# Optimization experiments

Measured on AMD Instinct MI355X. Metric: run time of the kernel, lower is better.

## Reference

```python
import jax, jax.numpy as jnp
import numpy as np

NEG_SLOPE = 0.2  # PyG GATConv default negative_slope


def gat_conv(x, edge_index, W, a_src, a_dst, b):
    """PyG GATConv with add_self_loops=True, concat=False (mean over heads).
    x: [N, F_in]; W: [F_in, H*D]; a_src/a_dst: [H, D]; b: [D].
    Returns [N, D].
    """
    N = x.shape[0]
    H, D = a_src.shape
    xh = (x @ W).reshape(N, H, D)            # [N, H, D]
    loop = jnp.arange(N, dtype=edge_index.dtype)
    src = jnp.concatenate([edge_index[0], loop])  # [E+N]
    dst = jnp.concatenate([edge_index[1], loop])  # [E+N]
    # per-node attention logits
    asrc = jnp.einsum('nhd,hd->nh', xh, a_src)    # [N, H]
    adst = jnp.einsum('nhd,hd->nh', xh, a_dst)    # [N, H]
    e = asrc[src] + adst[dst]                      # [E+N, H]
    e = jnp.where(e > 0, e, NEG_SLOPE * e)         # LeakyReLU
    # softmax over incoming edges of each destination node
    emax = jax.ops.segment_max(e, dst, num_segments=N)   # [N, H]
    ex = jnp.exp(e - emax[dst])
    denom = jax.ops.segment_sum(ex, dst, num_segments=N) # [N, H]
    alpha = ex / denom[dst]                               # [E+N, H]
    # scatter-aggregate messages
    out = jax.ops.segment_sum(alpha[:, :, None] * xh[src], dst, num_segments=N)  # [N, H, D]
    return out.mean(axis=1) + b                           # concat=False -> mean heads


def setup_inputs() -> dict:
    key = jax.random.key(0)
    ks = jax.random.split(key, 10)
    N, F, D, C, H, E = 100000, 128, 32, 16, 8, 1600000
    s1 = 1.0 / np.sqrt(F)
    s2 = 1.0 / np.sqrt(D)
    return {
        'x': jax.random.normal(ks[0], (N, F), dtype=jnp.float32),
        'edge_index': jax.random.randint(ks[1], (2, E), 0, N, dtype=jnp.int32),
        'W1': jax.random.normal(ks[2], (F, H * D), dtype=jnp.float32) * s1,
        'a_src1': jax.random.normal(ks[3], (H, D), dtype=jnp.float32) * s2,
        'a_dst1': jax.random.normal(ks[4], (H, D), dtype=jnp.float32) * s2,
        'b1': jnp.zeros((D,), dtype=jnp.float32),
        'W2': jax.random.normal(ks[5], (D, H * C), dtype=jnp.float32) * s2,
        'a_src2': jax.random.normal(ks[6], (H, C), dtype=jnp.float32) * (1.0 / np.sqrt(C)),
        'a_dst2': jax.random.normal(ks[7], (H, C), dtype=jnp.float32) * (1.0 / np.sqrt(C)),
        'b2': jnp.zeros((C,), dtype=jnp.float32),
    }


def reference(x, edge_index, W1, a_src1, a_dst1, b1, W2, a_src2, a_dst2, b2):
    h = gat_conv(x, edge_index, W1, a_src1, a_dst1, b1)
    h = jax.nn.elu(h)                       # F.elu; Dropout(p=0.0) is identity
    logits = gat_conv(h, edge_index, W2, a_src2, a_dst2, b2)
    return (jax.nn.log_softmax(logits, axis=1), logits)
```

## Files before the change

### kernel.cpp

```cpp
#include <hip/hip_runtime.h>
#include <hip/hip_bf16.h>
#include <hip/hip_fp16.h>
#include <math.h>

#define LEAK 0.2f
#define BSTRIDE 64

typedef _Float16 f16;
typedef _Float16 f16x2 __attribute__((ext_vector_type(2)));
typedef _Float16 f16x4 __attribute__((ext_vector_type(4)));
typedef _Float16 f16x8 __attribute__((ext_vector_type(8)));
typedef float f32x2 __attribute__((ext_vector_type(2)));
typedef float f32x4 __attribute__((ext_vector_type(4)));

__device__ inline unsigned char f32_to_fp8(float v) {
  int p = __builtin_amdgcn_cvt_pk_fp8_f32(v, v, 0, false);
  return (unsigned char)(p & 0xff);
}

__global__ void transpose_w_k(const float* __restrict__ W, f16* __restrict__ Wt,
                              int K, int NC) {
  int idx = blockIdx.x * 256 + threadIdx.x;
  if (idx >= K * NC) return;
  int n = idx / K, k = idx - n * K;
  Wt[idx] = (f16)W[(size_t)k * NC + n];
}

template <int K, int DH, bool FP8OUT, bool FILL>
__global__ __launch_bounds__(256) void gemm_att_mfma_k(
    const float* __restrict__ A, const f16* __restrict__ Bt,
    void* __restrict__ Cout, const float* __restrict__ a_src,
    const float* __restrict__ a_dst, float* __restrict__ asrc,
    float* __restrict__ adst, int M, int NC,
    const int* __restrict__ ei, int E, int Nn,
    unsigned* __restrict__ cnt, unsigned* __restrict__ bucket) {
  constexpr int CH = K / 8;
  __shared__ f16 As[64 * K];
  __shared__ f16 Bs[64 * K];
  const int tid = threadIdx.x;
  const int row0 = blockIdx.y * 64;
  const int col0 = blockIdx.x * 64;

#pragma unroll
  for (int it = 0; it < (64 * CH) / 256; ++it) {
    int idx = it * 256 + tid;
    int r = idx / CH, c = idx - r * CH;
    int grow = row0 + r;
    float4 v0 = make_float4(0.f, 0.f, 0.f, 0.f), v1 = v0;
    if (grow < M) {
      const float* gp = A + (size_t)grow * K + c * 8;
      v0 = *(const float4*)gp;
      v1 = *(const float4*)(gp + 4);
    }
    f16x8 h = {(f16)v0.x, (f16)v0.y, (f16)v0.z, (f16)v0.w,
               (f16)v1.x, (f16)v1.y, (f16)v1.z, (f16)v1.w};
    *(f16x8*)&As[r * K + (((c + r) & (CH - 1)) << 3)] = h;
  }
#pragma unroll
  for (int it = 0; it < (64 * CH) / 256; ++it) {
    int idx = it * 256 + tid;
    int n = idx / CH, c = idx - n * CH;
    f16x8 h = *(const f16x8*)(Bt + (size_t)(col0 + n) * K + c * 8);
    *(f16x8*)&Bs[n * K + (((c + n) & (CH - 1)) << 3)] = h;
  }
  __syncthreads();

  const int wv = tid >> 6;
  const int lane = tid & 63;
  const int l16 = lane & 15;
  const int l4 = lane >> 4;

  f32x4 acc[4];
#pragma unroll
  for (int ct = 0; ct < 4; ++ct) acc[ct] = (f32x4){0.f, 0.f, 0.f, 0.f};

  const int ar = wv * 16 + l16;
#pragma unroll
  for (int kt = 0; kt < K / 32; ++kt) {
    int aj = kt * 4 + l4;
    f16x8 av = *(const f16x8*)&As[ar * K + (((aj + ar) & (CH - 1)) << 3)];
#pragma unroll
    for (int ct = 0; ct < 4; ++ct) {
      int br = ct * 16 + l16;
      f16x8 bv = *(const f16x8*)&Bs[br * K + (((aj + br) & (CH - 1)) << 3)];
      acc[ct] = __builtin_amdgcn_mfma_f32_16x16x32_f16(av, bv, acc[ct], 0, 0, 0);
    }
  }

  constexpr int HPB = 64 / DH;
  constexpr int CTH = DH / 16;
  float ps[HPB][4], pd[HPB][4];
#pragma unroll
  for (int hl = 0; hl < HPB; ++hl)
#pragma unroll
    for (int r = 0; r < 4; ++r) { ps[hl][r] = 0.f; pd[hl][r] = 0.f; }

#pragma unroll
  for (int ct = 0; ct < 4; ++ct) {
    int col = col0 + ct * 16 + l16;
    float vs = a_src[col];
    float vd = a_dst[col];
    int hl = ct / CTH;
#pragma unroll
    for (int r = 0; r < 4; ++r) {
      ps[hl][r] += acc[ct][r] * vs;
      pd[hl][r] += acc[ct][r] * vd;
      int grow = row0 + wv * 16 + l4 * 4 + r;
      if (grow < M) {
        if (FP8OUT) {
          ((unsigned char*)Cout)[(size_t)grow * NC + col] = f32_to_fp8(acc[ct][r]);
        } else {
          ((f16*)Cout)[(size_t)grow * NC + col] = (f16)acc[ct][r];
        }
      }
    }
  }

#pragma unroll
  for (int hl = 0; hl < HPB; ++hl) {
#pragma unroll
    for (int r = 0; r < 4; ++r) {
      float s = ps[hl][r], d = pd[hl][r];
#pragma unroll
      for (int m = 1; m < 16; m <<= 1) {
        s += __shfl_xor(s, m, 64);
        d += __shfl_xor(d, m, 64);
      }
      if (l16 == 0) {
        int grow = row0 + wv * 16 + l4 * 4 + r;
        int h = (col0 / DH) + hl;
        if (grow < M) {
          asrc[(size_t)grow * 8 + h] = s;
          adst[(size_t)grow * 8 + h] = d;
        }
      }
    }
  }

  if (FILL) {
    const int nthreads = (int)(gridDim.x * gridDim.y) * 256;
    const int Mtot = E + Nn;
    for (int p = (int)(blockIdx.y * gridDim.x + blockIdx.x) * 256 + tid;
         p < Mtot; p += nthreads) {
      int s, d;
      if (p < E) {
        s = ei[p];
        d = ei[E + p];
      } else {
        s = d = p - E;
      }
      unsigned pos = atomicAdd(&cnt[d], 1u);
      if (pos < BSTRIDE)
        __builtin_nontemporal_store((unsigned)s, &bucket[((size_t)d << 6) + pos]);
    }
  }
}

__global__ __launch_bounds__(256) void aggregate1_k(const unsigned char* __restrict__ xh8,
                                                    const float* __restrict__ asrc,
                                                    const float* __restrict__ adst,
                                                    const unsigned* __restrict__ cnt,
                                                    const unsigned* __restrict__ bucket,
                                                    const float* __restrict__ b1,
                                                    float* __restrict__ hout, int N) {
  __shared__ float wlds[4][64][8];
  __shared__ unsigned slds[4][64];
  const int lane = threadIdx.x & 63;
  const int wv = threadIdx.x >> 6;
  const int n = blockIdx.x * 4 + wv;
  const int nn = n < N ? n : N - 1;
  int deg = (int)cnt[nn];
  deg = deg > BSTRIDE ? BSTRIDE : deg;
  unsigned sv = bucket[((size_t)nn << 6) + lane];
  if (lane >= deg) sv = 0;

  float w[8];
  if (lane < deg) {
    const float4* ap = (const float4*)(asrc + (size_t)sv * 8);
    const float4* bp = (const float4*)(adst + (size_t)nn * 8);
    float4 a0 = ap[0], a1 = ap[1];
    float4 b0 = bp[0], b1v = bp[1];
    float e[8] = {a0.x + b0.x, a0.y + b0.y, a0.z + b0.z, a0.w + b0.w,
                  a1.x + b1v.x, a1.y + b1v.y, a1.z + b1v.z, a1.w + b1v.w};
#pragma unroll
    for (int j = 0; j < 8; ++j) {
      float t = e[j];
      t = t > 0.f ? t : LEAK * t;
      w[j] = __expf(t);
    }
  } else {
#pragma unroll
    for (int j = 0; j < 8; ++j) w[j] = 0.f;
  }
  *(float4*)&wlds[wv][lane][0] = make_float4(w[0], w[1], w[2], w[3]);
  *(float4*)&wlds[wv][lane][4] = make_float4(w[4], w[5], w[6], w[7]);
  slds[wv][lane] = sv;
  __syncthreads();
  if (n >= N) return;

  const int sub = lane >> 5;
  const int sl = lane & 31;
  const int h = sl >> 2;
  const uint2* xw = (const uint2*)xh8;

  float a0 = 0.f, a1 = 0.f, a2 = 0.f, a3 = 0.f;
  float a4 = 0.f, a5 = 0.f, a6 = 0.f, a7 = 0.f;
  float dsum = 0.f;
#pragma unroll 4
  for (int i = 0; i < deg; i += 2) {
    float w8 = wlds[wv][i + sub][h];
    unsigned s = slds[wv][i + sub];
    uint2 b = xw[(size_t)s * 32 + sl];
    f32x2 p0 = __builtin_amdgcn_cvt_pk_f32_fp8(b.x, false);
    f32x2 p1 = __builtin_amdgcn_cvt_pk_f32_fp8(b.x, true);
    f32x2 p2 = __builtin_amdgcn_cvt_pk_f32_fp8(b.y, false);
    f32x2 p3 = __builtin_amdgcn_cvt_pk_f32_fp8(b.y, true);
    a0 += w8 * p0.x; a1 += w8 * p0.y; a2 += w8 * p1.x; a3 += w8 * p1.y;
    a4 += w8 * p2.x; a5 += w8 * p2.y; a6 += w8 * p3.x; a7 += w8 * p3.y;
    dsum += w8;
  }

  a0 += __shfl_xor(a0, 32, 64); a1 += __shfl_xor(a1, 32, 64);
  a2 += __shfl_xor(a2, 32, 64); a3 += __shfl_xor(a3, 32, 64);
  a4 += __shfl_xor(a4, 32, 64); a5 += __shfl_xor(a5, 32, 64);
  a6 += __shfl_xor(a6, 32, 64); a7 += __shfl_xor(a7, 32, 64);
  dsum += __shfl_xor(dsum, 32, 64);

  float rinv = 0.125f * __builtin_amdgcn_rcpf(dsum);
  a0 *= rinv; a1 *= rinv; a2 *= rinv; a3 *= rinv;
  a4 *= rinv; a5 *= rinv; a6 *= rinv; a7 *= rinv;

#pragma unroll
  for (int m = 16; m >= 4; m >>= 1) {
    a0 += __shfl_xor(a0, m, 64); a1 += __shfl_xor(a1, m, 64);
    a2 += __shfl_xor(a2, m, 64); a3 += __shfl_xor(a3, m, 64);
    a4 += __shfl_xor(a4, m, 64); a5 += __shfl_xor(a5, m, 64);
    a6 += __shfl_xor(a6, m, 64); a7 += __shfl_xor(a7, m, 64);
  }
  if (lane < 4) {
    int d = lane * 8;
    float4 bv0 = *(const float4*)(b1 + d);
    float4 bv1 = *(const float4*)(b1 + d + 4);
    float o0 = a0 + bv0.x, o1 = a1 + bv0.y, o2 = a2 + bv0.z, o3 = a3 + bv0.w;
    float o4 = a4 + bv1.x, o5 = a5 + bv1.y, o6 = a6 + bv1.z, o7 = a7 + bv1.w;
    o0 = o0 > 0.f ? o0 : expm1f(o0);
    o1 = o1 > 0.f ? o1 : expm1f(o1);
    o2 = o2 > 0.f ? o2 : expm1f(o2);
    o3 = o3 > 0.f ? o3 : expm1f(o3);
    o4 = o4 > 0.f ? o4 : expm1f(o4);
    o5 = o5 > 0.f ? o5 : expm1f(o5);
    o6 = o6 > 0.f ? o6 : expm1f(o6);
    o7 = o7 > 0.f ? o7 : expm1f(o7);
    *(float4*)(hout + (size_t)n * 32 + d) = make_float4(o0, o1, o2, o3);
    *(float4*)(hout + (size_t)n * 32 + d + 4) = make_float4(o4, o5, o6, o7);
  }
}

__global__ __launch_bounds__(256) void aggregate2_k(const unsigned char* __restrict__ xq,
                                                    const float* __restrict__ asrc,
                                                    const float* __restrict__ adst,
                                                    const unsigned* __restrict__ cnt,
                                                    const unsigned* __restrict__ bucket,
                                                    const float* __restrict__ b2,
                                                    float* __restrict__ out, int N) {
  __shared__ float wlds[4][64][8];
  __shared__ unsigned slds[4][64];
  const int lane = threadIdx.x & 63;
  const int wv = threadIdx.x >> 6;
  const int n = blockIdx.x * 4 + wv;
  const int nn = n < N ? n : N - 1;
  int deg = (int)cnt[nn];
  deg = deg > BSTRIDE ? BSTRIDE : deg;
  unsigned sv = bucket[((size_t)nn << 6) + lane];
  if (lane >= deg) sv = 0;

  float w[8];
  if (lane < deg) {
    const float4* ap = (const float4*)(asrc + (size_t)sv * 8);
    const float4* bp = (const float4*)(adst + (size_t)nn * 8);
    float4 a0 = ap[0], a1 = ap[1];
    float4 b0 = bp[0], b1v = bp[1];
    float e[8] = {a0.x + b0.x, a0.y + b0.y, a0.z + b0.z, a0.w + b0.w,
                  a1.x + b1v.x, a1.y + b1v.y, a1.z + b1v.z, a1.w + b1v.w};
#pragma unroll
    for (int j = 0; j < 8; ++j) {
      float t = e[j];
      t = t > 0.f ? t : LEAK * t;
      w[j] = __expf(t);
    }
  } else {
#pragma unroll
    for (int j = 0; j < 8; ++j) w[j] = 0.f;
  }
  *(float4*)&wlds[wv][lane][0] = make_float4(w[0], w[1], w[2], w[3]);
  *(float4*)&wlds[wv][lane][4] = make_float4(w[4], w[5], w[6], w[7]);
  slds[wv][lane] = sv;
  __syncthreads();
  if (n >= N) return;

  const int sub = lane >> 5;
  const int sl = lane & 31;
  const int h = sl >> 2;
  const unsigned* xw = (const unsigned*)xq;

  float a0 = 0.f, a1 = 0.f, a2 = 0.f, a3 = 0.f;
  float dsum = 0.f;
#pragma unroll 4
  for (int i = 0; i < deg; i += 2) {
    float w8 = wlds[wv][i + sub][h];
    unsigned s = slds[wv][i + sub];
    unsigned b = xw[(size_t)s * 32 + sl];
    f32x2 p0 = __builtin_amdgcn_cvt_pk_f32_fp8(b, false);
    f32x2 p1 = __builtin_amdgcn_cvt_pk_f32_fp8(b, true);
    a0 += w8 * p0.x; a1 += w8 * p0.y; a2 += w8 * p1.x; a3 += w8 * p1.y;
    dsum += w8;
  }

  a0 += __shfl_xor(a0, 32, 64); a1 += __shfl_xor(a1, 32, 64);
  a2 += __shfl_xor(a2, 32, 64); a3 += __shfl_xor(a3, 32, 64);
  dsum += __shfl_xor(dsum, 32, 64);

  float rinv = 0.125f * __builtin_amdgcn_rcpf(dsum);
  a0 *= rinv; a1 *= rinv; a2 *= rinv; a3 *= rinv;

#pragma unroll
  for (int m = 16; m >= 4; m >>= 1) {
    a0 += __shfl_xor(a0, m, 64); a1 += __shfl_xor(a1, m, 64);
    a2 += __shfl_xor(a2, m, 64); a3 += __shfl_xor(a3, m, 64);
  }
  int c = (lane & 3) * 4;
  float4 bv = *(const float4*)(b2 + c);
  float l0 = a0 + bv.x, l1 = a1 + bv.y, l2 = a2 + bv.z, l3 = a3 + bv.w;

  float mx = fmaxf(fmaxf(l0, l1), fmaxf(l2, l3));
  mx = fmaxf(mx, __shfl_xor(mx, 1, 64));
  mx = fmaxf(mx, __shfl_xor(mx, 2, 64));
  float es = __expf(l0 - mx) + __expf(l1 - mx) + __expf(l2 - mx) + __expf(l3 - mx);
  es += __shfl_xor(es, 1, 64);
  es += __shfl_xor(es, 2, 64);
  float lse = logf(es) + mx;

  if (lane < 4) {
    *(float4*)(out + (size_t)n * 16 + c) = make_float4(l0 - lse, l1 - lse, l2 - lse, l3 - lse);
    *(float4*)(out + (size_t)N * 16 + (size_t)n * 16 + c) = make_float4(l0, l1, l2, l3);
  }
}

extern "C" void kernel_launch(void* const* d_in, const int* in_sizes, int n_in,
                              void* d_out, int out_size, void* d_ws, size_t ws_size,
                              hipStream_t stream) {
  const float* x      = (const float*)d_in[0];
  const int*   ei     = (const int*)d_in[1];
  const float* W1     = (const float*)d_in[2];
  const float* a_src1 = (const float*)d_in[3];
  const float* a_dst1 = (const float*)d_in[4];
  const float* b1     = (const float*)d_in[5];
  const float* W2     = (const float*)d_in[6];
  const float* a_src2 = (const float*)d_in[7];
  const float* a_dst2 = (const float*)d_in[8];
  const float* b2     = (const float*)d_in[9];

  const int N = in_sizes[0] / 128;
  const int E = in_sizes[1] / 2;

  char* w = (char*)d_ws;
  size_t used = 0;
  auto alloc = [&](size_t bytes) -> void* {
    size_t aligned = (bytes + 255) & ~(size_t)255;
    void* p = w + used;
    used += aligned;
    return p;
  };
  unsigned char* xh1q = (unsigned char*)alloc((size_t)N * 256);
  unsigned char* xh2q = xh1q;
  float*    hbuf   = (float*)alloc((size_t)N * 32 * 4);
  float*    asrc   = (float*)alloc((size_t)N * 8 * 4);
  float*    adst   = (float*)alloc((size_t)N * 8 * 4);
  unsigned* cnt    = (unsigned*)alloc((size_t)N * 4);
  unsigned* bucket = (unsigned*)alloc((size_t)N * BSTRIDE * 4);
  f16*      w1t    = (f16*)alloc((size_t)128 * 256 * 2);
  f16*      w2t    = (f16*)alloc((size_t)32 * 128 * 2);
  (void)ws_size;

  float* out = (float*)d_out;
  const int gy = (N + 63) / 64;

  transpose_w_k<<<(128 * 256 + 255) / 256, 256, 0, stream>>>(W1, w1t, 128, 256);
  transpose_w_k<<<(32 * 128 + 255) / 256, 256, 0, stream>>>(W2, w2t, 32, 128);
  hipMemsetAsync(cnt, 0, (size_t)N * 4, stream);

  gemm_att_mfma_k<128, 32, true, true><<<dim3(4, gy), 256, 0, stream>>>(
      x, w1t, xh1q, a_src1, a_dst1, asrc, adst, N, 256, ei, E, N, cnt, bucket);

  aggregate1_k<<<(N + 3) / 4, 256, 0, stream>>>(xh1q, asrc, adst, cnt, bucket, b1, hbuf, N);

  gemm_att_mfma_k<32, 16, true, false><<<dim3(2, gy), 256, 0, stream>>>(
      hbuf, w2t, xh2q, a_src2, a_dst2, asrc, adst, N, 128, nullptr, 0, 0, nullptr, nullptr);
  aggregate2_k<<<(N + 3) / 4, 256, 0, stream>>>(xh2q, asrc, adst, cnt, bucket, b2, out, N);
}
```

Measured before the change: 386.4 us.

## Stage FP8 GEMM output through LDS for coalesced 16-byte stores and widen N tile

Each lane used to write scattered single fp8 bytes of the projected features straight to global memory. It now packs four fp8 values per lane, uses lane shuffles and byte permutes to assemble row-contiguous words, and stages them in a swizzled shared-memory buffer. The block then writes full 16-byte chunks per row. The column tile also grows from 64 to 128, halving the grid in x so each block reuses its A tile over more columns. The cost is an extra sync and a larger LDS footprint, which may reduce occupancy.

```diff
diff --git a/kernel.cpp b/kernel.cpp
--- a/kernel.cpp
+++ b/kernel.cpp
@@ -12,11 +12,6 @@
 typedef _Float16 f16x8 __attribute__((ext_vector_type(8)));
 typedef float f32x2 __attribute__((ext_vector_type(2)));
 typedef float f32x4 __attribute__((ext_vector_type(4)));
-
-__device__ inline unsigned char f32_to_fp8(float v) {
-  int p = __builtin_amdgcn_cvt_pk_fp8_f32(v, v, 0, false);
-  return (unsigned char)(p & 0xff);
-}
 
 __global__ void transpose_w_k(const float* __restrict__ W, f16* __restrict__ Wt,
                               int K, int NC) {
@@ -26,20 +21,23 @@
   Wt[idx] = (f16)W[(size_t)k * NC + n];
 }
 
-template <int K, int DH, bool FP8OUT, bool FILL>
+template <int K, int BN, int DH, bool FILL>
 __global__ __launch_bounds__(256) void gemm_att_mfma_k(
     const float* __restrict__ A, const f16* __restrict__ Bt,
-    void* __restrict__ Cout, const float* __restrict__ a_src,
+    unsigned char* __restrict__ Cout, const float* __restrict__ a_src,
     const float* __restrict__ a_dst, float* __restrict__ asrc,
     float* __restrict__ adst, int M, int NC,
     const int* __restrict__ ei, int E, int Nn,
     unsigned* __restrict__ cnt, unsigned* __restrict__ bucket) {
   constexpr int CH = K / 8;
-  __shared__ f16 As[64 * K];
-  __shared__ f16 Bs[64 * K];
+  constexpr int CT = BN / 16;
+  __shared__ __align__(16) unsigned char smem[(64 + BN) * K * 2];
+  f16* As = (f16*)smem;
+  f16* Bs = (f16*)(smem + 64 * K * 2);
+  unsigned char* stage = smem;
   const int tid = threadIdx.x;
   const int row0 = blockIdx.y * 64;
-  const int col0 = blockIdx.x * 64;
+  const int col0 = blockIdx.x * BN;
 
 #pragma unroll
   for (int it = 0; it < (64 * CH) / 256; ++it) {
@@ -57,7 +55,7 @@
     *(f16x8*)&As[r * K + (((c + r) & (CH - 1)) << 3)] = h;
   }
 #pragma unroll
-  for (int it = 0; it < (64 * CH) / 256; ++it) {
+  for (int it = 0; it < (BN * CH) / 256; ++it) {
     int idx = it * 256 + tid;
     int n = idx / CH, c = idx - n * CH;
     f16x8 h = *(const f16x8*)(Bt + (size_t)(col0 + n) * K + c * 8);
@@ -70,9 +68,9 @@
   const int l16 = lane & 15;
   const int l4 = lane >> 4;
 
-  f32x4 acc[4];
-#pragma unroll
-  for (int ct = 0; ct < 4; ++ct) acc[ct] = (f32x4){0.f, 0.f, 0.f, 0.f};
+  f32x4 acc[CT];
+#pragma unroll
+  for (int ct = 0; ct < CT; ++ct) acc[ct] = (f32x4){0.f, 0.f, 0.f, 0.f};
 
   const int ar = wv * 16 + l16;
 #pragma unroll
@@ -80,14 +78,14 @@
     int aj = kt * 4 + l4;
     f16x8 av = *(const f16x8*)&As[ar * K + (((aj + ar) & (CH - 1)) << 3)];
 #pragma unroll
-    for (int ct = 0; ct < 4; ++ct) {
+    for (int ct = 0; ct < CT; ++ct) {
       int br = ct * 16 + l16;
       f16x8 bv = *(const f16x8*)&Bs[br * K + (((aj + br) & (CH - 1)) << 3)];
       acc[ct] = __builtin_amdgcn_mfma_f32_16x16x32_f16(av, bv, acc[ct], 0, 0, 0);
     }
   }
 
-  constexpr int HPB = 64 / DH;
+  constexpr int HPB = BN / DH;
   constexpr int CTH = DH / 16;
   float ps[HPB][4], pd[HPB][4];
 #pragma unroll
@@ -96,7 +94,7 @@
     for (int r = 0; r < 4; ++r) { ps[hl][r] = 0.f; pd[hl][r] = 0.f; }
 
 #pragma unroll
-  for (int ct = 0; ct < 4; ++ct) {
+  for (int ct = 0; ct < CT; ++ct) {
     int col = col0 + ct * 16 + l16;
     float vs = a_src[col];
     float vd = a_dst[col];
@@ -105,14 +103,6 @@
     for (int r = 0; r < 4; ++r) {
       ps[hl][r] += acc[ct][r] * vs;
       pd[hl][r] += acc[ct][r] * vd;
-      int grow = row0 + wv * 16 + l4 * 4 + r;
-      if (grow < M) {
-        if (FP8OUT) {
-          ((unsigned char*)Cout)[(size_t)grow * NC + col] = f32_to_fp8(acc[ct][r]);
-        } else {
-          ((f16*)Cout)[(size_t)grow * NC + col] = (f16)acc[ct][r];
-        }
-      }
     }
   }
 
@@ -133,6 +123,47 @@
           asrc[(size_t)grow * 8 + h] = s;
           adst[(size_t)grow * 8 + h] = d;
         }
+      }
+    }
+  }
+
+  __syncthreads();
+  {
+    const int j = lane & 3;
+    const unsigned selAB = ((4u + j) << (8 * j)) | ((unsigned)j << (8 * (j ^ 1)));
+    const unsigned selCD = ((4u + j) << (8 * (j ^ 2))) | ((unsigned)j << (8 * (j ^ 3)));
+    const unsigned selMix =
+        0x03020100u + (0x04040404u & ((j & 2) ? 0xFFFF0000u : 0x0000FFFFu));
+    const int row = wv * 16 + l4 * 4 + j;
+    const int colq = (l16 >> 2) * 4;
+    const int swz = (row & 7) << 4;
+#pragma unroll
+    for (int ct = 0; ct < CT; ++ct) {
+      unsigned wpk = (unsigned)__builtin_amdgcn_cvt_pk_fp8_f32(
+          acc[ct][0], acc[ct][1], 0, false);
+      wpk = (unsigned)__builtin_amdgcn_cvt_pk_fp8_f32(
+          acc[ct][2], acc[ct][3], (int)wpk, true);
+      unsigned Bx = (unsigned)__shfl_xor((int)wpk, 1, 64);
+      unsigned Cx = (unsigned)__shfl_xor((int)wpk, 2, 64);
+      unsigned Dx = (unsigned)__shfl_xor((int)wpk, 3, 64);
+      unsigned P1 = __builtin_amdgcn_perm(wpk, Bx, selAB);
+      unsigned P2 = __builtin_amdgcn_perm(Cx, Dx, selCD);
+      unsigned ow = __builtin_amdgcn_perm(P1, P2, selMix);
+      int colb = ct * 16 + colq;
+      *(unsigned*)&stage[row * BN + (colb ^ swz)] = ow;
+    }
+  }
+  __syncthreads();
+  {
+    constexpr int CPR = BN / 16;
+#pragma unroll
+    for (int i = 0; i < (64 * CPR) / 256; ++i) {
+      int cid = i * 256 + tid;
+      int row = cid / CPR, ch = cid - row * CPR;
+      int grow = row0 + row;
+      if (grow < M) {
+        uint4 v = *(const uint4*)&stage[row * BN + ((ch * 16) ^ ((row & 7) << 4))];
+        *(uint4*)(Cout + (size_t)grow * NC + col0 + ch * 16) = v;
       }
     }
   }
@@ -389,12 +420,12 @@
   transpose_w_k<<<(32 * 128 + 255) / 256, 256, 0, stream>>>(W2, w2t, 32, 128);
   hipMemsetAsync(cnt, 0, (size_t)N * 4, stream);
 
-  gemm_att_mfma_k<128, 32, true, true><<<dim3(4, gy), 256, 0, stream>>>(
+  gemm_att_mfma_k<128, 128, 32, true><<<dim3(2, gy), 256, 0, stream>>>(
       x, w1t, xh1q, a_src1, a_dst1, asrc, adst, N, 256, ei, E, N, cnt, bucket);
 
   aggregate1_k<<<(N + 3) / 4, 256, 0, stream>>>(xh1q, asrc, adst, cnt, bucket, b1, hbuf, N);
 
-  gemm_att_mfma_k<32, 16, true, false><<<dim3(2, gy), 256, 0, stream>>>(
+  gemm_att_mfma_k<32, 128, 16, false><<<dim3(1, gy), 256, 0, stream>>>(
       hbuf, w2t, xh2q, a_src2, a_dst2, asrc, adst, N, 128, nullptr, 0, 0, nullptr, nullptr);
   aggregate2_k<<<(N + 3) / 4, 256, 0, stream>>>(xh2q, asrc, adst, cnt, bucket, b2, out, N);
 }
```

Result: slower. 401.3 us (+3.9%).
